# Optimization experiments

Hardware: AMD Instinct MI355X
Metric: run time of the kernel (lower is better)

Reference implementation:

```python
import jax, jax.numpy as jnp
import numpy as np


def setup_inputs() -> dict:
    key = jax.random.key(0)
    ks = jax.random.split(key, 11)
    B, N, C, E, O = 16, 2048, 64, 16, 64
    H, M, K = 16, 2, 2  # hyperGNN_dim, middle_dim, cheb_k
    s = 0.1
    return {
        "x": jax.random.normal(ks[0], (B, N, C), dtype=jnp.float32),
        "emb0": jax.random.normal(ks[1], (B, N, E), dtype=jnp.float32),
        "emb1": jax.random.normal(ks[2], (N, E), dtype=jnp.float32),
        "w1": jax.random.normal(ks[3], (C, H), dtype=jnp.float32) * s,
        "b1": jnp.zeros((H,), dtype=jnp.float32),
        "w2": jax.random.normal(ks[4], (H, M), dtype=jnp.float32) * s,
        "b2": jnp.zeros((M,), dtype=jnp.float32),
        "w3": jax.random.normal(ks[5], (M, E), dtype=jnp.float32) * s,
        "b3": jnp.zeros((E,), dtype=jnp.float32),
        "weights_pool": jax.random.normal(ks[6], (E, K, C, O), dtype=jnp.float32) * s,
        "bias_pool": jax.random.normal(ks[7], (E, O), dtype=jnp.float32) * s,
    }


def reference(x, emb0, emb1, w1, b1, w2, b2, w3, b3, weights_pool, bias_pool):
    # hypernetwork MLP: Linear -> sigmoid -> Linear -> sigmoid -> Linear
    h = jax.nn.sigmoid(x @ w1 + b1)
    h = jax.nn.sigmoid(h @ w2 + b2)
    filt = h @ w3 + b3                                   # (B,N,E)
    nodevec = jnp.tanh(emb0 * filt)                      # (B,N,E)
    # dynamic adjacency: relu(nodevec @ nodevec^T)
    adj = jax.nn.relu(jnp.einsum('bnd,bmd->bnm', nodevec, nodevec))  # (B,N,N)
    # normalized Laplacian: D^{-1/2} A D^{-1/2} (diag_embed expressed via broadcast)
    d = jnp.sum(adj, axis=-1) ** (-0.5)                  # (B,N)
    L = d[:, :, None] * adj * d[:, None, :]              # (B,N,N)
    # supports1 is identity -> x_g1 == x
    x_g1 = x
    x_g2 = jnp.einsum('bnm,bmc->bnc', L, x)
    x_g = jnp.stack([x_g1, x_g2], axis=2)                # (B,N,K=2,C)
    # per-node hypernetwork weights and bias
    weights = jnp.einsum('nd,dkio->nkio', emb1, weights_pool)  # (N,K,C,O)
    bias = emb1 @ bias_pool                               # (N,O)
    out = jnp.einsum('bnki,nkio->bno', x_g, weights) + bias
    return out
```

## Files before the change

### kernel.cpp

```cpp
#include <hip/hip_runtime.h>
#include <hip/hip_bf16.h>

#define B_ 16
#define N_ 2048
#define C_ 64
#define E_ 16
#define O_ 64
#define H_ 16

typedef __attribute__((ext_vector_type(8)))  short short8;
typedef __attribute__((ext_vector_type(16))) float f32x16;

#define NVB_OFF   0u
#define RSP_OFF   262144u
#define XST_OFF   393216u
#define YT_OFF    1441792u
#define XGALL_OFF 5636096u
#define WPB_OFF   7733248u
#define E1B_OFF   7799296u

__device__ __forceinline__ unsigned short f2bf(float f) {
  union { float f; unsigned int u; } v; v.f = f;
  unsigned int r = v.u + 0x7FFFu + ((v.u >> 16) & 1u);
  return (unsigned short)(r >> 16);
}
__device__ __forceinline__ float bf2f(unsigned short u) {
  union { unsigned int i; float f; } v; v.i = ((unsigned int)u) << 16;
  return v.f;
}

#define CVT_PK(dst, lo_, hi_) \
  asm("v_cvt_pk_bf16_f32 %0, %1, %2" : "=v"(dst) : "v"(lo_), "v"(hi_))
#define PL_SWAP(x_, y_) \
  asm("v_permlane32_swap_b32 %0, %1" : "+v"(x_), "+v"(y_))

__global__ __launch_bounds__(256) void k01_fused(
    const float* __restrict__ x, const float* __restrict__ emb0,
    const float* __restrict__ w1, const float* __restrict__ b1,
    const float* __restrict__ w2, const float* __restrict__ b2,
    const float* __restrict__ w3, const float* __restrict__ b3,
    const float* __restrict__ wp, const float* __restrict__ bp,
    const float* __restrict__ emb1,
    unsigned short* __restrict__ nvb, unsigned short* __restrict__ xgall,
    unsigned short* __restrict__ wpB, unsigned short* __restrict__ emb1b)
{
  int tid = threadIdx.x;
  if (blockIdx.x >= 128) {
    int id = (blockIdx.x - 128) * 256 + tid;
    if (id < 132096) {
      int t = id & 7, o = (id >> 3) & 63, rest = id >> 9;
      int sub = rest & 1, kc = rest >> 1;
      int q2 = sub * 8 + t;
      float v = (kc < 128) ? wp[(size_t)(kc * 16 + q2) * 64 + o]
                           : bp[(size_t)q2 * 64 + o];
      wpB[id] = f2bf(v);
    } else {
      int id2 = id - 132096;
      emb1b[id2] = f2bf(emb1[id2]);
    }
    return;
  }

  __shared__ float xt[128][65];
  __shared__ float w1s[C_*H_];
  __shared__ float b1s[H_], w2s[H_*2], b2s[2], w3s[2*E_], b3s[E_];
  for (int i = tid; i < C_*H_; i += 256) w1s[i] = w1[i];
  if (tid < H_)   b1s[tid] = b1[tid];
  if (tid < H_*2) w2s[tid] = w2[tid];
  if (tid < 2)    b2s[tid] = b2[tid];
  if (tid < 2*E_) w3s[tid] = w3[tid];
  if (tid < E_)   b3s[tid] = b3[tid];

  int base = blockIdx.x * 256;
  float xr[C_];
  #pragma unroll
  for (int ph = 0; ph < 2; ++ph) {
    const float4* src = reinterpret_cast<const float4*>(x + (size_t)(base + ph*128) * C_);
    #pragma unroll
    for (int j = 0; j < 8; ++j) {
      int i = j * 256 + tid;
      float4 v = src[i];
      int row = i >> 4, c4 = (i & 15) * 4;
      xt[row][c4]   = v.x; xt[row][c4+1] = v.y;
      xt[row][c4+2] = v.z; xt[row][c4+3] = v.w;
    }
    __syncthreads();
    if ((tid >> 7) == ph) {
      int lr = tid & 127;
      #pragma unroll
      for (int j = 0; j < C_; ++j) xr[j] = xt[lr][j];
    }
    __syncthreads();
  }

  int idx = base + tid;
  unsigned short xus[C_];
  #pragma unroll
  for (int c = 0; c < C_; ++c) xus[c] = f2bf(xr[c]);
  unsigned short* xo = xgall + (size_t)idx * 128;
  #pragma unroll
  for (int j = 0; j < 8; ++j)
    reinterpret_cast<uint4*>(xo)[j] = reinterpret_cast<uint4*>(xus)[j];

  float h1[H_];
  #pragma unroll
  for (int h = 0; h < H_; ++h) h1[h] = b1s[h];
  #pragma unroll 8
  for (int c = 0; c < C_; ++c) {
    float xv = xr[c];
    #pragma unroll
    for (int j = 0; j < 4; ++j) {
      float4 w = reinterpret_cast<const float4*>(&w1s[c*H_])[j];
      h1[4*j]   = fmaf(xv, w.x, h1[4*j]);
      h1[4*j+1] = fmaf(xv, w.y, h1[4*j+1]);
      h1[4*j+2] = fmaf(xv, w.z, h1[4*j+2]);
      h1[4*j+3] = fmaf(xv, w.w, h1[4*j+3]);
    }
  }
  #pragma unroll
  for (int h = 0; h < H_; ++h) h1[h] = 1.f / (1.f + __expf(-h1[h]));
  float a0 = b2s[0], a1 = b2s[1];
  #pragma unroll
  for (int h = 0; h < H_; ++h) {
    a0 = fmaf(h1[h], w2s[h*2],   a0);
    a1 = fmaf(h1[h], w2s[h*2+1], a1);
  }
  a0 = 1.f / (1.f + __expf(-a0));
  a1 = 1.f / (1.f + __expf(-a1));

  const float4* ep = reinterpret_cast<const float4*>(emb0 + (size_t)idx * E_);
  unsigned short us[E_];
  #pragma unroll
  for (int j = 0; j < 4; ++j) {
    float4 e = ep[j];
    int c = 4*j;
    us[c]   = f2bf(tanhf(e.x * (b3s[c]   + a0*w3s[c]   + a1*w3s[E_+c])));
    us[c+1] = f2bf(tanhf(e.y * (b3s[c+1] + a0*w3s[c+1] + a1*w3s[E_+c+1])));
    us[c+2] = f2bf(tanhf(e.z * (b3s[c+2] + a0*w3s[c+2] + a1*w3s[E_+c+2])));
    us[c+3] = f2bf(tanhf(e.w * (b3s[c+3] + a0*w3s[c+3] + a1*w3s[E_+c+3])));
  }
  *reinterpret_cast<short8*>(nvb + (size_t)idx * E_)     = *reinterpret_cast<short8*>(&us[0]);
  *reinterpret_cast<short8*>(nvb + (size_t)idx * E_ + 8) = *reinterpret_cast<short8*>(&us[8]);
}

__global__ __launch_bounds__(256, 4) void p1_rowsum(
    const unsigned short* __restrict__ nvb, float* __restrict__ rsp)
{
  int tid = threadIdx.x, lane = tid & 63, wid = tid >> 6;
  int lo = lane & 31, hi = lane >> 5;
  int orig = blockIdx.x;
  int eff = (orig & 7) * 128 + (orig >> 3);
  int rb = eff & 15, b = (eff >> 4) & 15, part = eff >> 8;
  int N0 = rb * 128 + wid * 32;

  short8 bfrag = *reinterpret_cast<const short8*>(
      nvb + ((size_t)b * N_ + N0 + lo) * E_ + 8 * hi);
  f32x16 zero = {};
  float rs = 0.f;
  const unsigned short* abase =
      nvb + ((size_t)b * N_ + part * 512 + lo) * E_ + 8 * hi;
  #pragma unroll 2
  for (int mc = 0; mc < 16; ++mc) {
    short8 afrag = *reinterpret_cast<const short8*>(abase + (size_t)mc * 32 * E_);
    f32x16 p = __builtin_amdgcn_mfma_f32_32x32x16_bf16(afrag, bfrag, zero, 0, 0, 0);
    #pragma unroll
    for (int r = 0; r < 16; ++r) rs += fmaxf(p[r], 0.f);
  }
  rs += __shfl_xor(rs, 32, 64);
  if (lane < 32) rsp[((size_t)part * B_ + b) * N_ + N0 + lo] = rs;
}

__global__ __launch_bounds__(256) void p2_scaleT(
    const float* __restrict__ x, const float* __restrict__ rsp,
    unsigned short* __restrict__ xsT)
{
  int tid = threadIdx.x;
  int c = tid & 63, g = tid >> 6;
  int m0 = blockIdx.x * 128 + g * 32;
  int b  = blockIdx.y;
  const float* rp = rsp + (size_t)b * N_;
  const size_t RST = (size_t)B_ * N_;
  unsigned int pk[16];
  #pragma unroll
  for (int k = 0; k < 32; ++k) {
    int m = m0 + k;
    float s = rp[m] + rp[RST + m] + rp[2*RST + m] + rp[3*RST + m];
    float d = rsqrtf(s);
    float v = d * x[((size_t)b * N_ + m) * C_ + c];
    unsigned short us = f2bf(v);
    if (k & 1) pk[k >> 1] |= ((unsigned int)us) << 16;
    else       pk[k >> 1]  = us;
  }
  unsigned short* o = xsT + (((size_t)b * 64 + (m0 >> 5)) * 64 + c) * 32;
  #pragma unroll
  for (int j = 0; j < 4; ++j)
    reinterpret_cast<uint4*>(o)[j] = *reinterpret_cast<uint4*>(&pk[4*j]);
}

__global__ __launch_bounds__(256, 4) void p3_spmm(
    const unsigned short* __restrict__ nvb, const unsigned short* __restrict__ xsT,
    unsigned short* __restrict__ yT)
{
  int tid = threadIdx.x, lane = tid & 63, wid = tid >> 6;
  int lo = lane & 31, hi = lane >> 5;
  int orig = blockIdx.x;
  int eff = (orig & 7) * 128 + (orig >> 3);
  int rb = eff & 15, b = (eff >> 4) & 15, part = eff >> 8;
  int N0 = rb * 128 + wid * 32;

  short8 bfrag = *reinterpret_cast<const short8*>(
      nvb + ((size_t)b * N_ + N0 + lo) * E_ + 8 * hi);
  f32x16 acc0 = {}, acc1 = {};
  f32x16 zero = {};
  const unsigned short* abase =
      nvb + ((size_t)b * N_ + part * 512 + lo) * E_ + 8 * hi;
  const unsigned short* xtile =
      xsT + (((size_t)b * 64 + part * 16) * 64) * 32 + lo * 32 + 8 * hi;

  #pragma unroll 2
  for (int mc = 0; mc < 16; ++mc) {
    short8 afrag = *reinterpret_cast<const short8*>(abase + (size_t)mc * 32 * E_);
    const unsigned short* xt = xtile + (size_t)mc * 2048;
    short8 x00 = *reinterpret_cast<const short8*>(xt);
    short8 x01 = *reinterpret_cast<const short8*>(xt + 16);
    short8 x10 = *reinterpret_cast<const short8*>(xt + 1024);
    short8 x11 = *reinterpret_cast<const short8*>(xt + 1024 + 16);

    f32x16 p = __builtin_amdgcn_mfma_f32_32x32x16_bf16(afrag, bfrag, zero, 0, 0, 0);
    float q[16];
    #pragma unroll
    for (int r = 0; r < 16; ++r) q[r] = fmaxf(p[r], 0.f);

    unsigned int A0, Bb0, C0, D0, A1, Bb1, C1, D1;
    CVT_PK(A0,  q[0],  q[1]);  CVT_PK(Bb0, q[2],  q[3]);
    CVT_PK(C0,  q[4],  q[5]);  CVT_PK(D0,  q[6],  q[7]);
    CVT_PK(A1,  q[8],  q[9]);  CVT_PK(Bb1, q[10], q[11]);
    CVT_PK(C1,  q[12], q[13]); CVT_PK(D1,  q[14], q[15]);
    PL_SWAP(A0, C0);  PL_SWAP(Bb0, D0);
    PL_SWAP(A1, C1);  PL_SWAP(Bb1, D1);

    union { unsigned int u[4]; short8 s; } f0, f1;
    f0.u[0] = A0; f0.u[1] = Bb0; f0.u[2] = C0; f0.u[3] = D0;
    f1.u[0] = A1; f1.u[1] = Bb1; f1.u[2] = C1; f1.u[3] = D1;

    acc0 = __builtin_amdgcn_mfma_f32_32x32x16_bf16(x00, f0.s, acc0, 0, 0, 0);
    acc0 = __builtin_amdgcn_mfma_f32_32x32x16_bf16(x01, f1.s, acc0, 0, 0, 0);
    acc1 = __builtin_amdgcn_mfma_f32_32x32x16_bf16(x10, f0.s, acc1, 0, 0, 0);
    acc1 = __builtin_amdgcn_mfma_f32_32x32x16_bf16(x11, f1.s, acc1, 0, 0, 0);
  }

  unsigned short* yb = yT + ((size_t)part * B_ + b) * C_ * N_;
  #pragma unroll
  for (int r = 0; r < 16; ++r) {
    int cl = (r & 3) + 8 * (r >> 2) + 4 * hi;
    yb[(size_t)cl * N_ + N0 + lo]        = f2bf(acc0[r]);
    yb[(size_t)(cl + 32) * N_ + N0 + lo] = f2bf(acc1[r]);
  }
}

__global__ __launch_bounds__(256) void p4_xg2(
    const unsigned short* __restrict__ yT, const float* __restrict__ rsp,
    unsigned short* __restrict__ xgall)
{
  __shared__ unsigned short tile[64][72];
  int tid = threadIdx.x;
  int nl = tid & 63, cg = tid >> 6;
  int n0 = blockIdx.x * 64, b = blockIdx.y;
  int n = n0 + nl;
  const size_t RST = (size_t)B_ * N_;
  float rs = rsp[(size_t)b * N_ + n]         + rsp[RST + (size_t)b * N_ + n]
           + rsp[2*RST + (size_t)b * N_ + n] + rsp[3*RST + (size_t)b * N_ + n];
  float dn = rsqrtf(rs);
  const unsigned short* y0 = yT + (size_t)b * C_ * N_;
  const size_t PST = (size_t)B_ * C_ * N_;
  #pragma unroll
  for (int cc = 0; cc < 16; cc += 2) {
    int c = cg * 16 + cc;
    size_t o0 = (size_t)c * N_ + n, o1 = (size_t)(c+1) * N_ + n;
    float v0 = bf2f(y0[o0]) + bf2f(y0[PST + o0]) + bf2f(y0[2*PST + o0]) + bf2f(y0[3*PST + o0]);
    float v1 = bf2f(y0[o1]) + bf2f(y0[PST + o1]) + bf2f(y0[2*PST + o1]) + bf2f(y0[3*PST + o1]);
    unsigned int pk = (unsigned int)f2bf(dn * v0) | ((unsigned int)f2bf(dn * v1) << 16);
    *reinterpret_cast<unsigned int*>(&tile[nl][c]) = pk;
  }
  __syncthreads();
  int q = tid & 3, j = tid >> 2;
  uint4 va = *reinterpret_cast<const uint4*>(&tile[j][q*16]);
  uint4 vb = *reinterpret_cast<const uint4*>(&tile[j][q*16 + 8]);
  unsigned short* o = xgall + ((size_t)b * N_ + n0 + j) * 128 + 64 + q * 16;
  *reinterpret_cast<uint4*>(o)     = va;
  *reinterpret_cast<uint4*>(o + 8) = vb;
}

__global__ __launch_bounds__(256) void k5_out(
    const unsigned short* __restrict__ xgall, const unsigned short* __restrict__ emb1b,
    const float* __restrict__ emb1, const unsigned short* __restrict__ wpB,
    float* __restrict__ out)
{
  int tid = threadIdx.x, lane = tid & 63, wid = tid >> 6;
  int lo = lane & 31, hi = lane >> 5;
  int gw = blockIdx.x * 4 + wid;
  int mt = gw >> 1;
  int o0 = (gw & 1) * 32;
  int M0 = mt * 32;
  int n0 = M0 & (N_ - 1);

  const unsigned short* arow = xgall + (size_t)(M0 + lo) * 128 + 8 * hi;
  short8 a[8];
  #pragma unroll
  for (int c8 = 0; c8 < 8; ++c8)
    a[c8] = *reinterpret_cast<const short8*>(arow + c8 * 16);
  short8 abias = *reinterpret_cast<const short8*>(
      emb1b + (size_t)(n0 + lo) * E_ + 8 * hi);

  f32x16 acc = {};
  f32x16 kzero = {};

  int nr[16];
  #pragma unroll
  for (int r = 0; r < 16; ++r) nr[r] = n0 + (r & 3) + 8 * (r >> 2) + 4 * hi;

  #pragma unroll 2
  for (int dg = 0; dg < 8; ++dg) {
    float2 e2[16];
    #pragma unroll
    for (int r = 0; r < 16; ++r)
      e2[r] = *reinterpret_cast<const float2*>(emb1 + (size_t)nr[r] * E_ + dg * 2);
    #pragma unroll
    for (int dd = 0; dd < 2; ++dd) {
      int d = dg * 2 + dd;
      const unsigned short* bbase = wpB + ((size_t)((d * 8) * 2 + hi) * 64 + o0 + lo) * 8;
      f32x16 t0 = kzero, t1 = kzero;
      #pragma unroll
      for (int c8 = 0; c8 < 8; c8 += 2) {
        short8 B0 = *reinterpret_cast<const short8*>(bbase + (size_t)(c8    ) * 1024);
        short8 B1 = *reinterpret_cast<const short8*>(bbase + (size_t)(c8 + 1) * 1024);
        t0 = __builtin_amdgcn_mfma_f32_32x32x16_bf16(a[c8],     B0, t0, 0, 0, 0);
        t1 = __builtin_amdgcn_mfma_f32_32x32x16_bf16(a[c8 + 1], B1, t1, 0, 0, 0);
      }
      #pragma unroll
      for (int r = 0; r < 16; ++r) {
        float e = dd ? e2[r].y : e2[r].x;
        acc[r] = fmaf(e, t0[r] + t1[r], acc[r]);
      }
    }
  }
  {
    const unsigned short* bbase = wpB + ((size_t)(256 + hi) * 64 + o0 + lo) * 8;
    short8 Bb = *reinterpret_cast<const short8*>(bbase);
    acc = __builtin_amdgcn_mfma_f32_32x32x16_bf16(abias, Bb, acc, 0, 0, 0);
  }
  #pragma unroll
  for (int r = 0; r < 16; ++r) {
    int cl = (r & 3) + 8 * (r >> 2) + 4 * hi;
    out[(size_t)(M0 + cl) * O_ + o0 + lo] = acc[r];
  }
}

extern "C" void kernel_launch(void* const* d_in, const int* in_sizes, int n_in,
                              void* d_out, int out_size, void* d_ws, size_t ws_size,
                              hipStream_t stream)
{
  const float* x    = (const float*)d_in[0];
  const float* emb0 = (const float*)d_in[1];
  const float* emb1 = (const float*)d_in[2];
  const float* w1   = (const float*)d_in[3];
  const float* b1   = (const float*)d_in[4];
  const float* w2   = (const float*)d_in[5];
  const float* b2   = (const float*)d_in[6];
  const float* w3   = (const float*)d_in[7];
  const float* b3   = (const float*)d_in[8];
  const float* wp   = (const float*)d_in[9];
  const float* bp   = (const float*)d_in[10];
  float* out = (float*)d_out;
  float* ws  = (float*)d_ws;

  unsigned short* nvb   = (unsigned short*)(ws + NVB_OFF);
  float*          rsp   = ws + RSP_OFF;
  unsigned short* xsT   = (unsigned short*)(ws + XST_OFF);
  unsigned short* yT    = (unsigned short*)(ws + YT_OFF);
  unsigned short* xgall = (unsigned short*)(ws + XGALL_OFF);
  unsigned short* wpB   = (unsigned short*)(ws + WPB_OFF);
  unsigned short* emb1b = (unsigned short*)(ws + E1B_OFF);

  k01_fused<<<772, 256, 0, stream>>>(x, emb0, w1, b1, w2, b2, w3, b3,
                                     wp, bp, emb1, nvb, xgall, wpB, emb1b);
  p1_rowsum<<<1024, 256, 0, stream>>>(nvb, rsp);
  p2_scaleT<<<dim3(16,16), 256, 0, stream>>>(x, rsp, xsT);
  p3_spmm  <<<1024, 256, 0, stream>>>(nvb, xsT, yT);
  p4_xg2   <<<dim3(32,16), 256, 0, stream>>>(yT, rsp, xgall);
  k5_out   <<<512, 256, 0, stream>>>(xgall, emb1b, emb1, wpB, out);
}
```

Before: 177.4 us.

## Coalesce weight repack, shrink scaleT per-thread work, move D^-1/2 into spmm, widen k5 MFMA chain

The weight-pool repack in k01 now stages a tile in shared memory so global reads are coalesced instead of strided. p2_scaleT gets four times as many blocks with eight rows per thread, giving more parallelism and fewer registers. The row scaling by d is applied in p3_spmm before the bf16 store, so p4 no longer reads rsp. k5_out runs four independent MFMA accumulators per loop iteration instead of two to expose more instruction-level parallelism. The cost is slightly more register pressure in k5, and rounding changes because the scale is now applied before the partial sums are reduced.

```diff
diff --git a/kernel.cpp b/kernel.cpp
--- a/kernel.cpp
+++ b/kernel.cpp
@@ -46,14 +46,22 @@
 {
   int tid = threadIdx.x;
   if (blockIdx.x >= 128) {
-    int id = (blockIdx.x - 128) * 256 + tid;
+    int bid = blockIdx.x - 128;
+    int id  = bid * 256 + tid;
     if (id < 132096) {
-      int t = id & 7, o = (id >> 3) & 63, rest = id >> 9;
-      int sub = rest & 1, kc = rest >> 1;
-      int q2 = sub * 8 + t;
-      float v = (kc < 128) ? wp[(size_t)(kc * 16 + q2) * 64 + o]
-                           : bp[(size_t)q2 * 64 + o];
-      wpB[id] = f2bf(v);
+      __shared__ float ls[8][68];
+      int sub = (bid >> 1) & 1, kc = bid >> 2;
+      const float* src = (kc < 128) ? (wp + (size_t)(kc * 16 + sub * 8) * 64)
+                                    : (bp + (size_t)sub * 8 * 64);
+      #pragma unroll
+      for (int j = 0; j < 2; ++j) {
+        int i2 = j * 256 + tid;
+        ls[i2 >> 6][i2 & 63] = src[i2];
+      }
+      __syncthreads();
+      int t = tid & 7;
+      int o = ((bid & 1) << 5) | (tid >> 3);
+      wpB[id] = f2bf(ls[t][o]);
     } else {
       int id2 = id - 132096;
       emb1b[id2] = f2bf(emb1[id2]);
@@ -176,13 +184,14 @@
 {
   int tid = threadIdx.x;
   int c = tid & 63, g = tid >> 6;
-  int m0 = blockIdx.x * 128 + g * 32;
+  int bx = blockIdx.x;
   int b  = blockIdx.y;
+  int m0 = bx * 32 + g * 8;
   const float* rp = rsp + (size_t)b * N_;
   const size_t RST = (size_t)B_ * N_;
-  unsigned int pk[16];
-  #pragma unroll
-  for (int k = 0; k < 32; ++k) {
+  unsigned int pk[4];
+  #pragma unroll
+  for (int k = 0; k < 8; ++k) {
     int m = m0 + k;
     float s = rp[m] + rp[RST + m] + rp[2*RST + m] + rp[3*RST + m];
     float d = rsqrtf(s);
@@ -191,15 +200,13 @@
     if (k & 1) pk[k >> 1] |= ((unsigned int)us) << 16;
     else       pk[k >> 1]  = us;
   }
-  unsigned short* o = xsT + (((size_t)b * 64 + (m0 >> 5)) * 64 + c) * 32;
-  #pragma unroll
-  for (int j = 0; j < 4; ++j)
-    reinterpret_cast<uint4*>(o)[j] = *reinterpret_cast<uint4*>(&pk[4*j]);
+  unsigned short* o = xsT + (((size_t)b * 64 + bx) * 64 + c) * 32 + g * 8;
+  *reinterpret_cast<uint4*>(o) = *reinterpret_cast<uint4*>(&pk[0]);
 }
 
 __global__ __launch_bounds__(256, 4) void p3_spmm(
     const unsigned short* __restrict__ nvb, const unsigned short* __restrict__ xsT,
-    unsigned short* __restrict__ yT)
+    const float* __restrict__ rsp, unsigned short* __restrict__ yT)
 {
   int tid = threadIdx.x, lane = tid & 63, wid = tid >> 6;
   int lo = lane & 31, hi = lane >> 5;
@@ -249,28 +256,27 @@
     acc1 = __builtin_amdgcn_mfma_f32_32x32x16_bf16(x11, f1.s, acc1, 0, 0, 0);
   }
 
+  const size_t RST = (size_t)B_ * N_;
+  const float* rpn = rsp + (size_t)b * N_ + N0 + lo;
+  float dn = rsqrtf(rpn[0] + rpn[RST] + rpn[2*RST] + rpn[3*RST]);
+
   unsigned short* yb = yT + ((size_t)part * B_ + b) * C_ * N_;
   #pragma unroll
   for (int r = 0; r < 16; ++r) {
     int cl = (r & 3) + 8 * (r >> 2) + 4 * hi;
-    yb[(size_t)cl * N_ + N0 + lo]        = f2bf(acc0[r]);
-    yb[(size_t)(cl + 32) * N_ + N0 + lo] = f2bf(acc1[r]);
+    yb[(size_t)cl * N_ + N0 + lo]        = f2bf(dn * acc0[r]);
+    yb[(size_t)(cl + 32) * N_ + N0 + lo] = f2bf(dn * acc1[r]);
   }
 }
 
 __global__ __launch_bounds__(256) void p4_xg2(
-    const unsigned short* __restrict__ yT, const float* __restrict__ rsp,
-    unsigned short* __restrict__ xgall)
+    const unsigned short* __restrict__ yT, unsigned short* __restrict__ xgall)
 {
   __shared__ unsigned short tile[64][72];
   int tid = threadIdx.x;
   int nl = tid & 63, cg = tid >> 6;
   int n0 = blockIdx.x * 64, b = blockIdx.y;
   int n = n0 + nl;
-  const size_t RST = (size_t)B_ * N_;
-  float rs = rsp[(size_t)b * N_ + n]         + rsp[RST + (size_t)b * N_ + n]
-           + rsp[2*RST + (size_t)b * N_ + n] + rsp[3*RST + (size_t)b * N_ + n];
-  float dn = rsqrtf(rs);
   const unsigned short* y0 = yT + (size_t)b * C_ * N_;
   const size_t PST = (size_t)B_ * C_ * N_;
   #pragma unroll
@@ -279,7 +285,7 @@
     size_t o0 = (size_t)c * N_ + n, o1 = (size_t)(c+1) * N_ + n;
     float v0 = bf2f(y0[o0]) + bf2f(y0[PST + o0]) + bf2f(y0[2*PST + o0]) + bf2f(y0[3*PST + o0]);
     float v1 = bf2f(y0[o1]) + bf2f(y0[PST + o1]) + bf2f(y0[2*PST + o1]) + bf2f(y0[3*PST + o1]);
-    unsigned int pk = (unsigned int)f2bf(dn * v0) | ((unsigned int)f2bf(dn * v1) << 16);
+    unsigned int pk = (unsigned int)f2bf(v0) | ((unsigned int)f2bf(v1) << 16);
     *reinterpret_cast<unsigned int*>(&tile[nl][c]) = pk;
   }
   __syncthreads();
@@ -325,24 +331,24 @@
     #pragma unroll
     for (int r = 0; r < 16; ++r)
       e2[r] = *reinterpret_cast<const float2*>(emb1 + (size_t)nr[r] * E_ + dg * 2);
-    #pragma unroll
-    for (int dd = 0; dd < 2; ++dd) {
-      int d = dg * 2 + dd;
-      const unsigned short* bbase = wpB + ((size_t)((d * 8) * 2 + hi) * 64 + o0 + lo) * 8;
-      f32x16 t0 = kzero, t1 = kzero;
-      #pragma unroll
-      for (int c8 = 0; c8 < 8; c8 += 2) {
-        short8 B0 = *reinterpret_cast<const short8*>(bbase + (size_t)(c8    ) * 1024);
-        short8 B1 = *reinterpret_cast<const short8*>(bbase + (size_t)(c8 + 1) * 1024);
-        t0 = __builtin_amdgcn_mfma_f32_32x32x16_bf16(a[c8],     B0, t0, 0, 0, 0);
-        t1 = __builtin_amdgcn_mfma_f32_32x32x16_bf16(a[c8 + 1], B1, t1, 0, 0, 0);
-      }
-      #pragma unroll
-      for (int r = 0; r < 16; ++r) {
-        float e = dd ? e2[r].y : e2[r].x;
-        acc[r] = fmaf(e, t0[r] + t1[r], acc[r]);
-      }
-    }
+    const unsigned short* bb0 = wpB + ((size_t)(dg * 32      + hi) * 64 + o0 + lo) * 8;
+    const unsigned short* bb1 = wpB + ((size_t)(dg * 32 + 16 + hi) * 64 + o0 + lo) * 8;
+    f32x16 t0a = kzero, t1a = kzero, t0b = kzero, t1b = kzero;
+    #pragma unroll
+    for (int c8 = 0; c8 < 8; c8 += 2) {
+      short8 B0a = *reinterpret_cast<const short8*>(bb0 + (size_t)(c8    ) * 1024);
+      short8 B1a = *reinterpret_cast<const short8*>(bb0 + (size_t)(c8 + 1) * 1024);
+      short8 B0b = *reinterpret_cast<const short8*>(bb1 + (size_t)(c8    ) * 1024);
+      short8 B1b = *reinterpret_cast<const short8*>(bb1 + (size_t)(c8 + 1) * 1024);
+      t0a = __builtin_amdgcn_mfma_f32_32x32x16_bf16(a[c8],     B0a, t0a, 0, 0, 0);
+      t1a = __builtin_amdgcn_mfma_f32_32x32x16_bf16(a[c8 + 1], B1a, t1a, 0, 0, 0);
+      t0b = __builtin_amdgcn_mfma_f32_32x32x16_bf16(a[c8],     B0b, t0b, 0, 0, 0);
+      t1b = __builtin_amdgcn_mfma_f32_32x32x16_bf16(a[c8 + 1], B1b, t1b, 0, 0, 0);
+    }
+    #pragma unroll
+    for (int r = 0; r < 16; ++r)
+      acc[r] = fmaf(e2[r].x, t0a[r] + t1a[r],
+               fmaf(e2[r].y, t0b[r] + t1b[r], acc[r]));
   }
   {
     const unsigned short* bbase = wpB + ((size_t)(256 + hi) * 64 + o0 + lo) * 8;
@@ -385,8 +391,8 @@
   k01_fused<<<772, 256, 0, stream>>>(x, emb0, w1, b1, w2, b2, w3, b3,
                                      wp, bp, emb1, nvb, xgall, wpB, emb1b);
   p1_rowsum<<<1024, 256, 0, stream>>>(nvb, rsp);
-  p2_scaleT<<<dim3(16,16), 256, 0, stream>>>(x, rsp, xsT);
-  p3_spmm  <<<1024, 256, 0, stream>>>(nvb, xsT, yT);
-  p4_xg2   <<<dim3(32,16), 256, 0, stream>>>(yT, rsp, xgall);
+  p2_scaleT<<<dim3(64,16), 256, 0, stream>>>(x, rsp, xsT);
+  p3_spmm  <<<1024, 256, 0, stream>>>(nvb, xsT, rsp, yT);
+  p4_xg2   <<<dim3(32,16), 256, 0, stream>>>(yT, xgall);
   k5_out   <<<512, 256, 0, stream>>>(xgall, emb1b, emb1, wpB, out);
 }
```

Measured after the change: 172.6 us. -2.7%, faster.
